# Optimization experiments

Measured on AMD Instinct MI355X. Metric: run time of the kernel, lower is better.

## Reference

```python
import jax, jax.numpy as jnp
import numpy as np

N, D, C = 8192, 10000, 1000


def setup_inputs() -> dict:
    key = jax.random.key(0)
    k1, k2 = jax.random.split(key)
    # binary {0,1} hypervectors, stored as float32 for efficient GEMM-form Hamming distance
    samples = jax.random.randint(k1, (N, D), 0, 2).astype(jnp.float32)
    classes_hv = jax.random.randint(k2, (C, D), 0, 2).astype(jnp.float32)
    return {"samples": samples, "classes_hv": classes_hv}


def reference(samples, classes_hv):
    # Original: response[i] = sum_d xor(samples[:, d], classes_hv[i, d])  (Hamming distance)
    # For binary a,b: xor(a,b) = a + b - 2*a*b, so the full [N, C] distance matrix is
    # dist = row_sum(samples)[:, None] + row_sum(hv)[None, :] - 2 * samples @ hv.T
    # This replaces the per-class XOR+reduce loop with one GEMM (same math).
    s_sum = jnp.sum(samples, axis=-1)          # [N]
    c_sum = jnp.sum(classes_hv, axis=-1)       # [C]
    cross = jnp.einsum('nd,cd->nc', samples, classes_hv)  # [N, C]
    return s_sum[:, None] + c_sum[None, :] - 2.0 * cross  # [N, C] Hamming distances
```

## Files before the change

### kernel.cpp

```cpp
#include <hip/hip_runtime.h>
#include <stdint.h>

#define N_ROWS 8192
#define C_CLS  1000
#define D_DIM  10000
#define W64P   160
#define W32P   (W64P * 2)
#define BKW    16
#define NCHUNK 20

typedef int v4i  __attribute__((ext_vector_type(4)));
typedef int v16i __attribute__((ext_vector_type(16)));

__global__ __launch_bounds__(256) void pack_kernel(
    const float* __restrict__ samples, const float* __restrict__ classes,
    unsigned long long* __restrict__ pA, unsigned long long* __restrict__ pB,
    uint32_t* __restrict__ rsA, uint32_t* __restrict__ rsB)
{
    int gwave = (blockIdx.x * 256 + threadIdx.x) >> 6;
    int lane  = threadIdx.x & 63;
    if (gwave >= N_ROWS + C_CLS) return;

    const float* src;
    unsigned long long* dst;
    uint32_t* rsw;
    if (gwave < N_ROWS) {
        src = samples + (size_t)gwave * D_DIM;
        dst = pA + (size_t)gwave * W64P;
        rsw = rsA + gwave;
    } else {
        int r = gwave - N_ROWS;
        src = classes + (size_t)r * D_DIM;
        dst = pB + (size_t)r * W64P;
        rsw = rsB + r;
    }

    uint32_t rs = 0;
    #pragma unroll 4
    for (int w = 0; w < 40; ++w) {
        int idx = w * 256 + lane * 4;
        float4 v = make_float4(0.f, 0.f, 0.f, 0.f);
        if (idx < D_DIM) v = *(const float4*)(src + idx);
        unsigned long long m0 = __ballot(v.x > 0.5f);
        unsigned long long m1 = __ballot(v.y > 0.5f);
        unsigned long long m2 = __ballot(v.z > 0.5f);
        unsigned long long m3 = __ballot(v.w > 0.5f);
        rs += (uint32_t)(__popcll(m0) + __popcll(m1) + __popcll(m2) + __popcll(m3));
        if (lane == 0) {
            uint4 p0, p1;
            p0.x = (uint32_t)m0; p0.y = (uint32_t)(m0 >> 32);
            p0.z = (uint32_t)m1; p0.w = (uint32_t)(m1 >> 32);
            p1.x = (uint32_t)m2; p1.y = (uint32_t)(m2 >> 32);
            p1.z = (uint32_t)m3; p1.w = (uint32_t)(m3 >> 32);
            *(uint4*)(dst + (size_t)w * 4)     = p0;
            *(uint4*)(dst + (size_t)w * 4 + 2) = p1;
        }
    }
    if (lane == 0) *rsw = rs;
}

__global__ __launch_bounds__(256) void hd_kernel(
    const uint32_t* __restrict__ pA, const uint32_t* __restrict__ pB,
    const uint32_t* __restrict__ rsA, const uint32_t* __restrict__ rsB,
    float* __restrict__ out)
{
    __shared__ uint32_t AsT[2][(BKW / 2) * 256];
    __shared__ uint32_t BsT[2][(BKW / 2) * 128];

    const int tid  = threadIdx.x;
    const int row0 = blockIdx.x * 128;
    const int col0 = blockIdx.y * 64;

    const int w    = tid >> 6;
    const int lane = tid & 63;
    const int wy   = w >> 1;
    const int wx   = w & 1;
    const int ln   = lane & 31;
    const int h4   = (lane >> 5) * 4;

    const int srow = tid >> 1;
    const int sq2  = (tid & 1) * 2;
    const uint32_t* gAs = pA + (size_t)(row0 + srow) * W32P + sq2 * 4;
    const int rb   = tid >> 2;
    const int qb   = tid & 3;
    int gc = col0 + rb; if (gc >= C_CLS) gc = C_CLS - 1;
    const uint32_t* gBs = pB + (size_t)gc * W32P + qb * 4;

    uint4 av[2], bv;

#define LOADR(ch) do {                                             \
    av[0] = *(const uint4*)(gAs + (ch) * BKW);                     \
    av[1] = *(const uint4*)(gAs + (ch) * BKW + 4);                 \
    bv    = *(const uint4*)(gBs + (ch) * BKW);                     \
} while (0)

#define WRITELDS(buf) do {                                         \
    uint32_t* ap_ = &AsT[buf][sq2 * 512 + srow * 2];               \
    *(uint2*)(ap_      ) = make_uint2(av[0].x, av[0].y);           \
    *(uint2*)(ap_ + 256) = make_uint2(av[0].z, av[0].w);           \
    *(uint2*)(ap_ + 512) = make_uint2(av[1].x, av[1].y);           \
    *(uint2*)(ap_ + 768) = make_uint2(av[1].z, av[1].w);           \
    uint32_t* bp_ = &BsT[buf][qb * 256 + rb * 2];                  \
    *(uint2*)(bp_      ) = make_uint2(bv.x, bv.y);                 \
    *(uint2*)(bp_ + 128) = make_uint2(bv.z, bv.w);                 \
} while (0)

#define UNP(dst, src) do {                                         \
    dst[0] = (int)(((src) >> (h4 + 0)) & 0x01010101u);             \
    dst[1] = (int)(((src) >> (h4 + 1)) & 0x01010101u);             \
    dst[2] = (int)(((src) >> (h4 + 2)) & 0x01010101u);             \
    dst[3] = (int)(((src) >> (h4 + 3)) & 0x01010101u);             \
} while (0)

    v16i acc0 = {}, acc1 = {};

    LOADR(0);
    WRITELDS(0);
    __syncthreads();

    #pragma unroll 2
    for (int ch = 0; ch < NCHUNK; ++ch) {
        const int cur = ch & 1;
        if (ch + 1 < NCHUNK) LOADR(ch + 1);

        const uint32_t* Ac = &AsT[cur][0];
        const uint32_t* Bc = &BsT[cur][0];

        #pragma unroll
        for (int p = 0; p < BKW / 2; ++p) {
            uint2 wa0 = *(const uint2*)&Ac[p * 256 + (wy * 64 + ln) * 2];
            uint2 wa1 = *(const uint2*)&Ac[p * 256 + (wy * 64 + 32 + ln) * 2];
            uint2 wb  = *(const uint2*)&Bc[p * 128 + (wx * 32 + ln) * 2];
            v4i a0, a1, b;
            UNP(a0, wa0.x); UNP(a1, wa1.x); UNP(b, wb.x);
            acc0 = __builtin_amdgcn_mfma_i32_32x32x32_i8(a0, b, acc0, 0, 0, 0);
            acc1 = __builtin_amdgcn_mfma_i32_32x32x32_i8(a1, b, acc1, 0, 0, 0);
            UNP(a0, wa0.y); UNP(a1, wa1.y); UNP(b, wb.y);
            acc0 = __builtin_amdgcn_mfma_i32_32x32x32_i8(a0, b, acc0, 0, 0, 0);
            acc1 = __builtin_amdgcn_mfma_i32_32x32x32_i8(a1, b, acc1, 0, 0, 0);
        }

        if (ch + 1 < NCHUNK) {
            WRITELDS((ch + 1) & 1);
            __syncthreads();
        }
    }
#undef LOADR
#undef WRITELDS
#undef UNP

    const int gcol = col0 + wx * 32 + ln;
    const uint32_t rbv = (gcol < C_CLS) ? rsB[gcol] : 0u;
    if (gcol < C_CLS) {
        #pragma unroll
        for (int r = 0; r < 16; ++r) {
            const int m    = (r & 3) + 8 * (r >> 2) + h4;
            const int rowa = row0 + wy * 64 + m;
            const int rowb = rowa + 32;
            out[(size_t)rowa * C_CLS + gcol] =
                (float)(int)(rsA[rowa] + rbv - 2u * (uint32_t)acc0[r]);
            out[(size_t)rowb * C_CLS + gcol] =
                (float)(int)(rsA[rowb] + rbv - 2u * (uint32_t)acc1[r]);
        }
    }
}

extern "C" void kernel_launch(void* const* d_in, const int* in_sizes, int n_in,
                              void* d_out, int out_size, void* d_ws, size_t ws_size,
                              hipStream_t stream) {
    const float* samples = (const float*)d_in[0];
    const float* classes = (const float*)d_in[1];
    float* out = (float*)d_out;

    unsigned long long* pA = (unsigned long long*)d_ws;
    unsigned long long* pB = pA + (size_t)N_ROWS * W64P;
    uint32_t* rsA = (uint32_t*)(pB + (size_t)C_CLS * W64P);
    uint32_t* rsB = rsA + N_ROWS;

    int waves  = N_ROWS + C_CLS;
    int blocks = (waves + 3) / 4;
    pack_kernel<<<blocks, 256, 0, stream>>>(samples, classes, pA, pB, rsA, rsB);

    dim3 grid(N_ROWS / 128, 16);
    hd_kernel<<<grid, 256, 0, stream>>>((const uint32_t*)pA, (const uint32_t*)pB,
                                        rsA, rsB, out);
}
```

Before: 543.8 us.

## Split K across waves with k-major repacked bits and LDS reduction

```diff
diff --git a/kernel.cpp b/kernel.cpp
--- a/kernel.cpp
+++ b/kernel.cpp
@@ -3,11 +3,13 @@
 
 #define N_ROWS 8192
 #define C_CLS  1000
+#define C_PAD  1024
 #define D_DIM  10000
 #define W64P   160
 #define W32P   (W64P * 2)
-#define BKW    16
-#define NCHUNK 20
+#define GS     (32 * W32P)
+#define KWPW   80
+#define NSS    20
 
 typedef int v4i  __attribute__((ext_vector_type(4)));
 typedef int v16i __attribute__((ext_vector_type(16)));
@@ -59,50 +61,71 @@
     if (lane == 0) *rsw = rs;
 }
 
+__global__ __launch_bounds__(256) void repack_kernel(
+    const uint32_t* __restrict__ srcA, const uint32_t* __restrict__ srcB,
+    uint32_t* __restrict__ dstA, uint32_t* __restrict__ dstB)
+{
+    const int g  = blockIdx.x;
+    const int t  = threadIdx.x;
+    const int r  = t & 31;
+    const int wq = t >> 5;
+
+    const uint32_t* src;
+    uint32_t* dst;
+    int srow;
+    bool valid;
+    if (g < 256) {
+        src = srcA; dst = dstA + (size_t)g * GS;
+        srow = g * 32 + r; valid = true;
+    } else {
+        int gb = g - 256;
+        src = srcB; dst = dstB + (size_t)gb * GS;
+        srow = gb * 32 + r; valid = (srow < C_CLS);
+    }
+
+    #pragma unroll
+    for (int i = 0; i < 10; ++i) {
+        int wb = (i * 8 + wq) * 4;
+        uint4 v = make_uint4(0u, 0u, 0u, 0u);
+        if (valid) v = *(const uint4*)&src[(size_t)srow * W32P + wb];
+        dst[(size_t)(wb + 0) * 32 + r] = v.x;
+        dst[(size_t)(wb + 1) * 32 + r] = v.y;
+        dst[(size_t)(wb + 2) * 32 + r] = v.z;
+        dst[(size_t)(wb + 3) * 32 + r] = v.w;
+    }
+}
+
 __global__ __launch_bounds__(256) void hd_kernel(
-    const uint32_t* __restrict__ pA, const uint32_t* __restrict__ pB,
+    const uint32_t* __restrict__ Akm, const uint32_t* __restrict__ Bkm,
     const uint32_t* __restrict__ rsA, const uint32_t* __restrict__ rsB,
     float* __restrict__ out)
 {
-    __shared__ uint32_t AsT[2][(BKW / 2) * 256];
-    __shared__ uint32_t BsT[2][(BKW / 2) * 128];
+    __shared__ int red[64 * 65];
 
     const int tid  = threadIdx.x;
-    const int row0 = blockIdx.x * 128;
-    const int col0 = blockIdx.y * 64;
-
     const int w    = tid >> 6;
     const int lane = tid & 63;
-    const int wy   = w >> 1;
-    const int wx   = w & 1;
     const int ln   = lane & 31;
     const int h4   = (lane >> 5) * 4;
-
-    const int srow = tid >> 1;
-    const int sq2  = (tid & 1) * 2;
-    const uint32_t* gAs = pA + (size_t)(row0 + srow) * W32P + sq2 * 4;
-    const int rb   = tid >> 2;
-    const int qb   = tid & 3;
-    int gc = col0 + rb; if (gc >= C_CLS) gc = C_CLS - 1;
-    const uint32_t* gBs = pB + (size_t)gc * W32P + qb * 4;
-
-    uint4 av[2], bv;
-
-#define LOADR(ch) do {                                             \
-    av[0] = *(const uint4*)(gAs + (ch) * BKW);                     \
-    av[1] = *(const uint4*)(gAs + (ch) * BKW + 4);                 \
-    bv    = *(const uint4*)(gBs + (ch) * BKW);                     \
-} while (0)
-
-#define WRITELDS(buf) do {                                         \
-    uint32_t* ap_ = &AsT[buf][sq2 * 512 + srow * 2];               \
-    *(uint2*)(ap_      ) = make_uint2(av[0].x, av[0].y);           \
-    *(uint2*)(ap_ + 256) = make_uint2(av[0].z, av[0].w);           \
-    *(uint2*)(ap_ + 512) = make_uint2(av[1].x, av[1].y);           \
-    *(uint2*)(ap_ + 768) = make_uint2(av[1].z, av[1].w);           \
-    uint32_t* bp_ = &BsT[buf][qb * 256 + rb * 2];                  \
-    *(uint2*)(bp_      ) = make_uint2(bv.x, bv.y);                 \
-    *(uint2*)(bp_ + 128) = make_uint2(bv.z, bv.w);                 \
+    const int rt   = blockIdx.x;
+    const int ct   = blockIdx.y;
+
+    const uint32_t* A0 = Akm + (size_t)(2 * rt) * GS;
+    const uint32_t* A1 = A0 + GS;
+    const uint32_t* B0 = Bkm + (size_t)(2 * ct) * GS;
+    const uint32_t* B1 = B0 + GS;
+    int o = w * (KWPW * 32) + ln;
+
+    uint32_t a0w[2][4], a1w[2][4], b0w[2][4], b1w[2][4];
+
+#define LOADSS(s, oo) do {                                         \
+    _Pragma("unroll")                                              \
+    for (int k_ = 0; k_ < 4; ++k_) {                               \
+        a0w[s][k_] = A0[(oo) + k_ * 32];                           \
+        a1w[s][k_] = A1[(oo) + k_ * 32];                           \
+        b0w[s][k_] = B0[(oo) + k_ * 32];                           \
+        b1w[s][k_] = B1[(oo) + k_ * 32];                           \
+    }                                                              \
 } while (0)
 
 #define UNP(dst, src) do {                                         \
@@ -112,56 +135,63 @@
     dst[3] = (int)(((src) >> (h4 + 3)) & 0x01010101u);             \
 } while (0)
 
-    v16i acc0 = {}, acc1 = {};
-
-    LOADR(0);
-    WRITELDS(0);
-    __syncthreads();
+    v16i acc00 = {}, acc01 = {}, acc10 = {}, acc11 = {};
+
+    LOADSS(0, o);
 
     #pragma unroll 2
-    for (int ch = 0; ch < NCHUNK; ++ch) {
-        const int cur = ch & 1;
-        if (ch + 1 < NCHUNK) LOADR(ch + 1);
-
-        const uint32_t* Ac = &AsT[cur][0];
-        const uint32_t* Bc = &BsT[cur][0];
+    for (int ss = 0; ss < NSS; ++ss) {
+        const int cur = ss & 1;
+        if (ss + 1 < NSS) LOADSS(cur ^ 1, o + 128);
 
         #pragma unroll
-        for (int p = 0; p < BKW / 2; ++p) {
-            uint2 wa0 = *(const uint2*)&Ac[p * 256 + (wy * 64 + ln) * 2];
-            uint2 wa1 = *(const uint2*)&Ac[p * 256 + (wy * 64 + 32 + ln) * 2];
-            uint2 wb  = *(const uint2*)&Bc[p * 128 + (wx * 32 + ln) * 2];
-            v4i a0, a1, b;
-            UNP(a0, wa0.x); UNP(a1, wa1.x); UNP(b, wb.x);
-            acc0 = __builtin_amdgcn_mfma_i32_32x32x32_i8(a0, b, acc0, 0, 0, 0);
-            acc1 = __builtin_amdgcn_mfma_i32_32x32x32_i8(a1, b, acc1, 0, 0, 0);
-            UNP(a0, wa0.y); UNP(a1, wa1.y); UNP(b, wb.y);
-            acc0 = __builtin_amdgcn_mfma_i32_32x32x32_i8(a0, b, acc0, 0, 0, 0);
-            acc1 = __builtin_amdgcn_mfma_i32_32x32x32_i8(a1, b, acc1, 0, 0, 0);
+        for (int k = 0; k < 4; ++k) {
+            v4i a0f, a1f, b0f, b1f;
+            UNP(a0f, a0w[cur][k]); UNP(b0f, b0w[cur][k]);
+            acc00 = __builtin_amdgcn_mfma_i32_32x32x32_i8(a0f, b0f, acc00, 0, 0, 0);
+            UNP(b1f, b1w[cur][k]);
+            acc01 = __builtin_amdgcn_mfma_i32_32x32x32_i8(a0f, b1f, acc01, 0, 0, 0);
+            UNP(a1f, a1w[cur][k]);
+            acc10 = __builtin_amdgcn_mfma_i32_32x32x32_i8(a1f, b0f, acc10, 0, 0, 0);
+            acc11 = __builtin_amdgcn_mfma_i32_32x32x32_i8(a1f, b1f, acc11, 0, 0, 0);
         }
-
-        if (ch + 1 < NCHUNK) {
-            WRITELDS((ch + 1) & 1);
-            __syncthreads();
+        o += 128;
+    }
+#undef LOADSS
+#undef UNP
+
+    #pragma unroll
+    for (int p = 0; p < 4; ++p) {
+        if (w == p) {
+            #pragma unroll
+            for (int r = 0; r < 16; ++r) {
+                const int m = (r & 3) + 8 * (r >> 2) + h4;
+                if (p == 0) {
+                    red[m * 65 + ln]             = acc00[r];
+                    red[m * 65 + 32 + ln]        = acc01[r];
+                    red[(m + 32) * 65 + ln]      = acc10[r];
+                    red[(m + 32) * 65 + 32 + ln] = acc11[r];
+                } else {
+                    red[m * 65 + ln]             += acc00[r];
+                    red[m * 65 + 32 + ln]        += acc01[r];
+                    red[(m + 32) * 65 + ln]      += acc10[r];
+                    red[(m + 32) * 65 + 32 + ln] += acc11[r];
+                }
+            }
         }
-    }
-#undef LOADR
-#undef WRITELDS
-#undef UNP
-
-    const int gcol = col0 + wx * 32 + ln;
+        __syncthreads();
+    }
+
+    const int gcol = ct * 64 + lane;
     const uint32_t rbv = (gcol < C_CLS) ? rsB[gcol] : 0u;
-    if (gcol < C_CLS) {
-        #pragma unroll
-        for (int r = 0; r < 16; ++r) {
-            const int m    = (r & 3) + 8 * (r >> 2) + h4;
-            const int rowa = row0 + wy * 64 + m;
-            const int rowb = rowa + 32;
-            out[(size_t)rowa * C_CLS + gcol] =
-                (float)(int)(rsA[rowa] + rbv - 2u * (uint32_t)acc0[r]);
-            out[(size_t)rowb * C_CLS + gcol] =
-                (float)(int)(rsA[rowb] + rbv - 2u * (uint32_t)acc1[r]);
-        }
+    #pragma unroll
+    for (int i = 0; i < 16; ++i) {
+        const int row  = w * 16 + i;
+        const int grow = rt * 64 + row;
+        const int v    = red[row * 65 + lane];
+        if (gcol < C_CLS)
+            out[(size_t)grow * C_CLS + gcol] =
+                (float)(int)(rsA[grow] + rbv - 2u * (uint32_t)v);
     }
 }
 
@@ -172,16 +202,20 @@
     const float* classes = (const float*)d_in[1];
     float* out = (float*)d_out;
 
-    unsigned long long* pA = (unsigned long long*)d_ws;
-    unsigned long long* pB = pA + (size_t)N_ROWS * W64P;
-    uint32_t* rsA = (uint32_t*)(pB + (size_t)C_CLS * W64P);
-    uint32_t* rsB = rsA + N_ROWS;
+    uint32_t* pArm = (uint32_t*)d_ws;
+    uint32_t* pBrm = pArm + (size_t)N_ROWS * W32P;
+    uint32_t* pAkm = pBrm + (size_t)C_CLS * W32P;
+    uint32_t* pBkm = pAkm + (size_t)N_ROWS * W32P;
+    uint32_t* rsA  = pBkm + (size_t)C_PAD * W32P;
+    uint32_t* rsB  = rsA + N_ROWS;
 
     int waves  = N_ROWS + C_CLS;
     int blocks = (waves + 3) / 4;
-    pack_kernel<<<blocks, 256, 0, stream>>>(samples, classes, pA, pB, rsA, rsB);
-
-    dim3 grid(N_ROWS / 128, 16);
-    hd_kernel<<<grid, 256, 0, stream>>>((const uint32_t*)pA, (const uint32_t*)pB,
-                                        rsA, rsB, out);
-}
+    pack_kernel<<<blocks, 256, 0, stream>>>(samples, classes,
+        (unsigned long long*)pArm, (unsigned long long*)pBrm, rsA, rsB);
+
+    repack_kernel<<<288, 256, 0, stream>>>(pArm, pBrm, pAkm, pBkm);
+
+    dim3 grid(N_ROWS / 64, C_PAD / 64);
+    hd_kernel<<<grid, 256, 0, stream>>>(pAkm, pBkm, rsA, rsB, out);
+}
```

Result: slower. 560.1 us (+3.0%).
